# Optimization experiments

Hardware: AMD Instinct MI355X
Metric: run time of the kernel (lower is better)

Reference implementation:

```python
import jax, jax.numpy as jnp
import numpy as np

THRESH = 0.5   # global `thresh` used by ActFun
LENS = 0.5     # global `lens` (surrogate width)
DECAY = 0.25   # LIFNode init_decay
INV_STD = 1.0 / float(np.sqrt(1.0 + 1e-5))  # BN eval: running_mean=0, running_var=1
HEADS = 8
WINDOW = 8

@jax.custom_vjp
def act_fun(x):
    return (x > THRESH).astype(x.dtype)

def _act_fwd(x):
    return act_fun(x), x

def _act_bwd(x, g):
    temp = (jnp.abs(x - THRESH) < LENS).astype(g.dtype) / (2.0 * LENS)
    return (g * temp,)

act_fun.defvjp(_act_fwd, _act_bwd)

def lif(x):
    # x: [T, ...]; mem = x[0]; mem_t = mem_{t-1}*decay*(1-spike_{t-1}.detach()) + x_t
    spike0 = act_fun(x[0])
    def step(carry, xi):
        mem_prev, spike_prev = carry
        mem = mem_prev * DECAY * (1.0 - jax.lax.stop_gradient(spike_prev)) + xi
        spike = act_fun(mem)
        return (mem, spike), spike
    _, spikes = jax.lax.scan(step, (x[0], spike0), x[1:])
    return jnp.concatenate([spike0[None], spikes], axis=0)

def bn_eval(x, gamma, beta):
    # BatchNorm2d eval over channel D (last dim of [T,B,L,D]) with default running stats
    return x * (INV_STD * gamma) + beta

def linear(x, w, b):
    # torch nn.Linear: y = x @ w.T + b, w: [out, in]
    return jnp.einsum('tbld,ed->tble', x, w) + b


def setup_inputs() -> dict:
    key = jax.random.key(0)
    ks = jax.random.split(key, 12)
    T, B, L, D = 4, 4, 1024, 512
    s = 0.02
    inp = {
        'x': jax.random.normal(ks[0], (T, B, L, D), dtype=jnp.float32),
        'pos_bias': jax.random.uniform(ks[1], (L, L), dtype=jnp.float32),
        'q_w': jax.random.normal(ks[2], (D, D), dtype=jnp.float32) * s,
        'q_b': jnp.zeros((D,), jnp.float32),
        'q_g': jnp.ones((D,), jnp.float32),
        'q_beta': jnp.zeros((D,), jnp.float32),
        'k_w': jax.random.normal(ks[3], (D, D), dtype=jnp.float32) * s,
        'k_b': jnp.zeros((D,), jnp.float32),
        'k_g': jnp.ones((D,), jnp.float32),
        'k_beta': jnp.zeros((D,), jnp.float32),
        'v_w': jax.random.normal(ks[4], (D, D), dtype=jnp.float32) * s,
        'v_b': jnp.zeros((D,), jnp.float32),
        'v_g': jnp.ones((D,), jnp.float32),
        'v_beta': jnp.zeros((D,), jnp.float32),
        'last_w': jax.random.normal(ks[5], (D, D), dtype=jnp.float32) * s,
        'last_b': jnp.zeros((D,), jnp.float32),
        'last_g': jnp.ones((D,), jnp.float32),
        'last_beta': jnp.zeros((D,), jnp.float32),
    }
    return inp


def reference(x, pos_bias, q_w, q_b, q_g, q_beta, k_w, k_b, k_g, k_beta,
              v_w, v_b, v_g, v_beta, last_w, last_b, last_g, last_beta):
    T, B, L, D = x.shape
    H = HEADS
    Dh = D // H
    # local causal band: keep pos_bias[i,j] only where 0 <= i-j < WINDOW
    i = jnp.arange(L)[:, None]
    j = jnp.arange(L)[None, :]
    band = ((i - j) >= 0) & ((i - j) < WINDOW)
    pb = jnp.where(band, pos_bias[:L, :L], 0.0)  # [L, L]

    xs = lif(x)  # first_lif
    q = lif(bn_eval(linear(xs, q_w, q_b), q_g, q_beta))
    k = lif(bn_eval(linear(xs, k_w, k_b), k_g, k_beta))
    v = lif(bn_eval(linear(xs, v_w, v_b), v_g, v_beta))

    # [T,B,L,D] -> [T,B,L,H,Dh] -> [B,H,L,T,Dh] -> [B,H,L,T*Dh]
    qh = q.reshape(T, B, L, H, Dh).transpose(1, 3, 2, 0, 4).reshape(B, H, L, T * Dh)
    kv = (k * v).reshape(T, B, L, H, Dh).transpose(1, 3, 2, 0, 4).reshape(B, H, L, T * Dh)

    attn = jnp.einsum('ij,bhjd->bhid', pb, kv)  # local-window positional mixing
    out = qh * attn
    out = out.reshape(B, H, L, T, Dh).transpose(3, 0, 2, 1, 4).reshape(T, B, L, D)
    out = lif(out)  # attn_lif
    out = bn_eval(linear(out, last_w, last_b), last_g, last_beta)
    return out
```

## Files before the change

kernel.cpp:

```cpp
#include <hip/hip_runtime.h>
#include <stdint.h>


#define T_ 4
#define B_ 4
#define L_ 1024
#define D_ 512
#define BI_ (B_*L_)
#define M_ROWS (T_*B_*L_)
#define STRIDE4 (B_*L_*D_/4)
#define INV_STD 0.9999950000374997f
#define EPS_FLAG 1e-3f
#define LIST_CAP 5000000u

typedef unsigned int   u32;
typedef unsigned short u16;
typedef __bf16 bf16x8 __attribute__((ext_vector_type(8)));
typedef float  f32x4  __attribute__((ext_vector_type(4)));

static __device__ __forceinline__ float spike_of(float m) {
  return m > 0.5f ? 1.0f : 0.0f;
}
static __device__ __forceinline__ u16 sbits(float s) {
  return s != 0.0f ? (u16)0x3F80 : (u16)0;
}

__device__ __forceinline__ void gll16(const u16* g, void* l) {
  __builtin_amdgcn_global_load_lds(
      (const __attribute__((address_space(1))) u32*)(const void*)g,
      (__attribute__((address_space(3))) u32*)l, 16, 0, 0);
}

__global__ __launch_bounds__(256) void k_wsplit(const float* __restrict__ qw,
    const float* __restrict__ kw, const float* __restrict__ vw,
    const float* __restrict__ lw, u16* __restrict__ wsp, u32* __restrict__ cnt) {
  int idx = blockIdx.x * 256 + threadIdx.x;
  if (idx == 0) *cnt = 0;
  int mat = idx >> 16;
  int u = idx & 65535;
  const float* W = mat == 0 ? qw : mat == 1 ? kw : mat == 2 ? vw : lw;
  float4 w = ((const float4*)W)[u];
  float wv[4] = {w.x, w.y, w.z, w.w};
  u16 hb[4], lb[4];
#pragma unroll
  for (int c = 0; c < 4; ++c) {
    __bf16 h = (__bf16)wv[c];
    float r = wv[c] - (float)h;
    __bf16 lo = (__bf16)r;
    hb[c] = __builtin_bit_cast(u16, h);
    lb[c] = __builtin_bit_cast(u16, lo);
  }
  u16* base = wsp + (size_t)mat * 524288;
  ((ushort4*)base)[u]            = make_ushort4(hb[0], hb[1], hb[2], hb[3]);
  ((ushort4*)(base + 262144))[u] = make_ushort4(lb[0], lb[1], lb[2], lb[3]);
}

__global__ __launch_bounds__(256) void k_lif_first(const float* __restrict__ x,
                                                   u16* __restrict__ xsb) {
  int idx = blockIdx.x * 256 + threadIdx.x;
  if (idx >= STRIDE4) return;
  const int bi = idx >> 7, d4 = idx & 127;
  const float4* x4 = (const float4*)x;
  ushort4* o4 = (ushort4*)xsb;
  float m[4], s[4];
  float4 v = x4[idx];
  m[0] = v.x; m[1] = v.y; m[2] = v.z; m[3] = v.w;
#pragma unroll
  for (int c = 0; c < 4; ++c) s[c] = spike_of(m[c]);
  o4[(bi * 4 + 0) * 128 + d4] =
      make_ushort4(sbits(s[0]), sbits(s[1]), sbits(s[2]), sbits(s[3]));
#pragma unroll
  for (int t = 1; t < T_; ++t) {
    v = x4[idx + t * STRIDE4];
    float xv[4] = {v.x, v.y, v.z, v.w};
#pragma unroll
    for (int c = 0; c < 4; ++c) {
      m[c] = m[c] * 0.25f * (1.0f - s[c]) + xv[c];
      s[c] = spike_of(m[c]);
    }
    o4[(bi * 4 + t) * 128 + d4] =
        make_ushort4(sbits(s[0]), sbits(s[1]), sbits(s[2]), sbits(s[3]));
  }
}

__device__ __forceinline__ void gemm_core(const u16* __restrict__ Ab,
    const u16* __restrict__ Wp, int row0, int col0, int tid,
    unsigned char* sm, f32x4 (&acc)[4][4]) {
  const u16* gsrc[12];
  int loff[12];
#pragma unroll
  for (int u = 0; u < 12; ++u) {
    if (u < 4) {
      int lin = u * 4096 + tid * 16;
      int r = lin >> 7, slot = (lin >> 4) & 7, gs = slot ^ (r & 7);
      gsrc[u] = Ab + (size_t)(row0 + r) * 512 + gs * 8;
      loff[u] = lin;
    } else {
      int lin = (u - 4) * 4096 + tid * 16;
      int plane = lin >> 14, l3 = lin & 16383;
      int r = l3 >> 7, slot = (l3 >> 4) & 7, gs = slot ^ (r & 7);
      gsrc[u] = Wp + (size_t)plane * 262144 + (size_t)(col0 + r) * 512 + gs * 8;
      loff[u] = 16384 + lin;
    }
  }
  const int lane = tid & 63;
  const int wid = tid >> 6;
  const int wr = wid >> 1, wc = wid & 1;
  const int la = lane & 15, lg = lane >> 4;

  int offA[4][2], offB[2][4][2];
#pragma unroll
  for (int mi = 0; mi < 4; ++mi) {
    int r = wr * 64 + mi * 16 + la;
#pragma unroll
    for (int s = 0; s < 2; ++s)
      offA[mi][s] = r * 128 + ((s * 64 + lg * 16) ^ ((r & 7) << 4));
  }
#pragma unroll
  for (int p = 0; p < 2; ++p)
#pragma unroll
    for (int ni = 0; ni < 4; ++ni) {
      int r = wc * 64 + ni * 16 + la;
#pragma unroll
      for (int s = 0; s < 2; ++s)
        offB[p][ni][s] = 16384 + p * 16384 + r * 128 +
                         ((s * 64 + lg * 16) ^ ((r & 7) << 4));
    }

#pragma unroll
  for (int a = 0; a < 4; ++a)
#pragma unroll
    for (int b = 0; b < 4; ++b) acc[a][b] = (f32x4){0.f, 0.f, 0.f, 0.f};

  for (int k0 = 0; k0 < 8; ++k0) {
#pragma unroll
    for (int u = 0; u < 12; ++u) gll16(gsrc[u] + (k0 << 6), sm + loff[u]);
    __syncthreads();
    uint4 af[4][2];
#pragma unroll
    for (int mi = 0; mi < 4; ++mi)
#pragma unroll
      for (int s = 0; s < 2; ++s)
        af[mi][s] = *(const uint4*)(sm + offA[mi][s]);
#pragma unroll
    for (int p = 0; p < 2; ++p)
#pragma unroll
      for (int s = 0; s < 2; ++s)
#pragma unroll
        for (int ni = 0; ni < 4; ++ni) {
          uint4 bf = *(const uint4*)(sm + offB[p][ni][s]);
#pragma unroll
          for (int mi = 0; mi < 4; ++mi)
            acc[mi][ni] = __builtin_amdgcn_mfma_f32_16x16x32_bf16(
                __builtin_bit_cast(bf16x8, af[mi][s]),
                __builtin_bit_cast(bf16x8, bf), acc[mi][ni], 0, 0, 0);
        }
    __syncthreads();
  }
}

__global__ __launch_bounds__(256) void k_gemm_lif(const u16* __restrict__ Ab,
    const u16* __restrict__ Wp, const float* __restrict__ bias,
    const float* __restrict__ gamma, const float* __restrict__ beta,
    u16* __restrict__ S, u32* __restrict__ list, u32* __restrict__ cnt,
    int tz) {
  __shared__ __align__(16) unsigned char sm[49152];
  const int tid = threadIdx.x;
  int f = blockIdx.y * 4 + blockIdx.x;
  int tI = (f & 7) * 64 + (f >> 3);
  const int row0 = (tI >> 2) * 128;
  const int col0 = (tI & 3) * 128;

  f32x4 acc[4][4];
  gemm_core(Ab, Wp, row0, col0, tid, sm, acc);

  const int lane = tid & 63;
  const int wid = tid >> 6;
  const int wr = wid >> 1, wc = wid & 1;
  const int la = lane & 15, lg = lane >> 4;

#pragma unroll
  for (int ni = 0; ni < 4; ++ni) {
    int e = col0 + wc * 64 + ni * 16 + la;
    float cs = INV_STD * gamma[e];
    float cb = bias[e], ct = beta[e];
#pragma unroll
    for (int mi = 0; mi < 4; ++mi) {
      int r = row0 + wr * 64 + mi * 16 + lg * 4;
      int bi = r >> 2;
      float m = 0.f, s = 0.f;
      int fl = 0;
      u16 sb[4];
#pragma unroll
      for (int p = 0; p < 4; ++p) {
        float pre = (acc[mi][ni][p] + cb) * cs + ct;
        if (p == 0) m = pre;
        else m = m * 0.25f * (1.0f - s) + pre;
        s = spike_of(m);
        if (fabsf(m - 0.5f) < EPS_FLAG) fl = 1;
        sb[p] = sbits(s);
      }
#pragma unroll
      for (int p = 0; p < 4; ++p)
        S[(size_t)(r + p) * 512 + e] = sb[p];
      if (fl) {
        u32 pos = atomicAdd(cnt, 1u);
        if (pos < LIST_CAP)
          list[pos] = ((u32)tz << 21) | (u32)(bi * 512 + e);
      }
    }
  }
}

__global__ __launch_bounds__(256) void k_gemm_out(const u16* __restrict__ Ab,
    const u16* __restrict__ Wp, const float* __restrict__ bias,
    const float* __restrict__ gamma, const float* __restrict__ beta,
    float* __restrict__ Y) {
  __shared__ __align__(16) unsigned char sm[49152];
  const int tid = threadIdx.x;
  int f = blockIdx.y * 4 + blockIdx.x;
  int tI = (f & 7) * 64 + (f >> 3);
  const int row0 = (tI >> 2) * 128;
  const int col0 = (tI & 3) * 128;

  f32x4 acc[4][4];
  gemm_core(Ab, Wp, row0, col0, tid, sm, acc);

  const int lane = tid & 63;
  const int wid = tid >> 6;
  const int wr = wid >> 1, wc = wid & 1;
  const int la = lane & 15, lg = lane >> 4;

#pragma unroll
  for (int ni = 0; ni < 4; ++ni) {
    int e = col0 + wc * 64 + ni * 16 + la;
    float cs = INV_STD * gamma[e];
    float cb = bias[e], ct = beta[e];
#pragma unroll
    for (int mi = 0; mi < 4; ++mi) {
      int r = row0 + wr * 64 + mi * 16 + lg * 4;
      int bi = r >> 2;
#pragma unroll
      for (int p = 0; p < 4; ++p)
        Y[(size_t)(p * BI_ + bi) * 512 + e] = (acc[mi][ni][p] + cb) * cs + ct;
    }
  }
}

__device__ __forceinline__ void consume32_1(const float4 (&wb)[8],
                                            const uint4 (&ab)[4], float& c) {
#pragma unroll
  for (int u = 0; u < 8; ++u) {
    float4 w = wb[u];
    uint4 tt = ab[u >> 1];
    u32 a = (u & 1) ? tt.z : tt.x, b = (u & 1) ? tt.w : tt.y;
    c += (a & 0xFFFFu) ? w.x : 0.0f;
    c += (a >> 16)     ? w.y : 0.0f;
    c += (b & 0xFFFFu) ? w.z : 0.0f;
    c += (b >> 16)     ? w.w : 0.0f;
  }
}

__global__ __launch_bounds__(128) void k_fixup_c(const u16* __restrict__ xsb,
    u16* __restrict__ qs, u16* __restrict__ ks, u16* __restrict__ vs,
    const float* __restrict__ qw, const float* __restrict__ qb2,
    const float* __restrict__ qg, const float* __restrict__ qbe,
    const float* __restrict__ kw, const float* __restrict__ kb2,
    const float* __restrict__ kg, const float* __restrict__ kbe,
    const float* __restrict__ vw, const float* __restrict__ vb2,
    const float* __restrict__ vg, const float* __restrict__ vbe,
    const u32* __restrict__ list, const u32* __restrict__ cnt) {
  u32 n = *cnt;
  if (n > LIST_CAP) n = LIST_CAP;
  u32 tot = n * 4;
  for (u32 ii = blockIdx.x * 128 + threadIdx.x; ii < tot;
       ii += gridDim.x * 128) {
    u32 i = ii >> 2;
    int t = (int)(ii & 3);
    u32 e = list[i];
    int tz = (int)(e >> 21);
    int col = (int)(e & 0x1FFFFFu);
    int bi = col >> 9, d = col & 511;
    const float* W  = tz == 0 ? qw  : tz == 1 ? kw  : vw;
    const float* Bb = tz == 0 ? qb2 : tz == 1 ? kb2 : vb2;
    const float* Gg = tz == 0 ? qg  : tz == 1 ? kg  : vg;
    const float* Be = tz == 0 ? qbe : tz == 1 ? kbe : vbe;
    u16* S          = tz == 0 ? qs  : tz == 1 ? ks  : vs;
    const float4* w4 = (const float4*)(W + (size_t)d * 512);
    const uint4*  R  = (const uint4*)(xsb + ((size_t)bi * 4 + t) * 512);

    float4 wA[8], wB[8];
    uint4 aA[4], aB[4];
#pragma unroll
    for (int u = 0; u < 8; ++u) wA[u] = w4[u];
#pragma unroll
    for (int u = 0; u < 4; ++u) aA[u] = R[u];
    float c = 0.f;
#pragma unroll
    for (int ch = 0; ch < 16; ++ch) {
      if ((ch & 1) == 0) {
        if (ch + 1 < 16) {
          int wb0 = (ch + 1) * 8, ab0 = (ch + 1) * 4;
#pragma unroll
          for (int u = 0; u < 8; ++u) wB[u] = w4[wb0 + u];
#pragma unroll
          for (int u = 0; u < 4; ++u) aB[u] = R[ab0 + u];
        }
        consume32_1(wA, aA, c);
      } else {
        if (ch + 1 < 16) {
          int wb0 = (ch + 1) * 8, ab0 = (ch + 1) * 4;
#pragma unroll
          for (int u = 0; u < 8; ++u) wA[u] = w4[wb0 + u];
#pragma unroll
          for (int u = 0; u < 4; ++u) aA[u] = R[ab0 + u];
        }
        consume32_1(wB, aB, c);
      }
    }
    int lane = threadIdx.x & 63;
    int qb = lane & ~3;
    float cq[4];
    cq[0] = __shfl(c, qb + 0, 64);
    cq[1] = __shfl(c, qb + 1, 64);
    cq[2] = __shfl(c, qb + 2, 64);
    cq[3] = __shfl(c, qb + 3, 64);
    float cs = INV_STD * Gg[d];
    float cb = Bb[d], ct = Be[d];
    float m = 0.f, s = 0.f;
    u16 myb = 0;
#pragma unroll
    for (int t2 = 0; t2 < 4; ++t2) {
      float pre = (cq[t2] + cb) * cs + ct;
      if (t2 == 0) m = pre;
      else m = m * 0.25f * (1.0f - s) + pre;
      s = spike_of(m);
      if (t2 == t) myb = sbits(s);
    }
    S[((size_t)bi * 4 + t) * 512 + d] = myb;
  }
}

__global__ __launch_bounds__(256) void k_attn(const u16* __restrict__ qs,
    const u16* __restrict__ ks, const u16* __restrict__ vs,
    const float* __restrict__ pos_bias, u16* __restrict__ sout) {
  int idx = blockIdx.x * 256 + threadIdx.x;
  if (idx >= STRIDE4) return;
  const int d4 = idx & 127;
  const int bi = idx >> 7;
  const int i = bi & (L_ - 1);
  const int wmax = i < 7 ? i : 7;

  float pbv[8];
  const float* pbrow = pos_bias + (size_t)i * L_ + i;
  for (int w = 0; w <= wmax; ++w) pbv[w] = pbrow[-w];

  const ushort4* k4 = (const ushort4*)ks;
  const ushort4* v4 = (const ushort4*)vs;
  const ushort4* q4 = (const ushort4*)qs;
  float pre[T_][4];

#pragma unroll
  for (int t = 0; t < T_; ++t) {
    float sum[4] = {0.f, 0.f, 0.f, 0.f};
    for (int w = wmax; w >= 0; --w) {
      int rj = ((bi - w) * 4 + t) * 128 + d4;
      ushort4 ku = k4[rj];
      ushort4 vu = v4[rj];
      sum[0] += (ku.x && vu.x) ? pbv[w] : 0.0f;
      sum[1] += (ku.y && vu.y) ? pbv[w] : 0.0f;
      sum[2] += (ku.z && vu.z) ? pbv[w] : 0.0f;
      sum[3] += (ku.w && vu.w) ? pbv[w] : 0.0f;
    }
    ushort4 qu = q4[(bi * 4 + t) * 128 + d4];
    pre[t][0] = qu.x ? sum[0] : 0.0f;
    pre[t][1] = qu.y ? sum[1] : 0.0f;
    pre[t][2] = qu.z ? sum[2] : 0.0f;
    pre[t][3] = qu.w ? sum[3] : 0.0f;
  }

  ushort4* s4 = (ushort4*)sout;
  float m[4], s[4];
#pragma unroll
  for (int c = 0; c < 4; ++c) { m[c] = pre[0][c]; s[c] = spike_of(m[c]); }
  s4[(bi * 4 + 0) * 128 + d4] =
      make_ushort4(sbits(s[0]), sbits(s[1]), sbits(s[2]), sbits(s[3]));
#pragma unroll
  for (int t = 1; t < T_; ++t) {
#pragma unroll
    for (int c = 0; c < 4; ++c) {
      m[c] = m[c] * 0.25f * (1.0f - s[c]) + pre[t][c];
      s[c] = spike_of(m[c]);
    }
    s4[(bi * 4 + t) * 128 + d4] =
        make_ushort4(sbits(s[0]), sbits(s[1]), sbits(s[2]), sbits(s[3]));
  }
}

extern "C" void kernel_launch(void* const* d_in, const int* in_sizes, int n_in,
                              void* d_out, int out_size, void* d_ws, size_t ws_size,
                              hipStream_t stream) {
  (void)in_sizes; (void)n_in; (void)out_size; (void)ws_size;
  const float* x        = (const float*)d_in[0];
  const float* pos_bias = (const float*)d_in[1];
  const float* q_w    = (const float*)d_in[2];
  const float* q_b    = (const float*)d_in[3];
  const float* q_g    = (const float*)d_in[4];
  const float* q_beta = (const float*)d_in[5];
  const float* k_w    = (const float*)d_in[6];
  const float* k_b    = (const float*)d_in[7];
  const float* k_g    = (const float*)d_in[8];
  const float* k_beta = (const float*)d_in[9];
  const float* v_w    = (const float*)d_in[10];
  const float* v_b    = (const float*)d_in[11];
  const float* v_g    = (const float*)d_in[12];
  const float* v_beta = (const float*)d_in[13];
  const float* last_w    = (const float*)d_in[14];
  const float* last_b    = (const float*)d_in[15];
  const float* last_g    = (const float*)d_in[16];
  const float* last_beta = (const float*)d_in[17];
  float* out = (float*)d_out;

  char* ws = (char*)d_ws;
  u16*   xsb  = (u16*)(ws + 0);
  u16*   qs   = (u16*)(ws + 16777216);
  u16*   ks   = (u16*)(ws + 33554432);
  u16*   vs   = (u16*)(ws + 50331648);
  u16*   sA   = (u16*)(ws + 67108864);
  u16*   wsp  = (u16*)(ws + 100663296);
  u32*   list = (u32*)(ws + 104857600);
  u32*   cnt  = (u32*)(ws + 124857600);

  dim3 gg(4, 128);

  k_wsplit<<<1024, 256, 0, stream>>>(q_w, k_w, v_w, last_w, wsp, cnt);
  k_lif_first<<<2048, 256, 0, stream>>>(x, xsb);

  k_gemm_lif<<<gg, 256, 0, stream>>>(xsb, wsp + 0 * 524288, q_b, q_g, q_beta,
                                     qs, list, cnt, 0);
  k_gemm_lif<<<gg, 256, 0, stream>>>(xsb, wsp + 1 * 524288, k_b, k_g, k_beta,
                                     ks, list, cnt, 1);
  k_gemm_lif<<<gg, 256, 0, stream>>>(xsb, wsp + 2 * 524288, v_b, v_g, v_beta,
                                     vs, list, cnt, 2);

  k_fixup_c<<<2048, 128, 0, stream>>>(xsb, qs, ks, vs,
      q_w, q_b, q_g, q_beta, k_w, k_b, k_g, k_beta, v_w, v_b, v_g, v_beta,
      list, cnt);

  k_attn<<<2048, 256, 0, stream>>>(qs, ks, vs, pos_bias, sA);

  k_gemm_out<<<gg, 256, 0, stream>>>(sA, wsp + 3 * 524288,
                                     last_b, last_g, last_beta, out);
}
```

Before: 366.5 us.

## Merge Q/K/V GEMM launches and stage epilogue stores through LDS for coalescing

```diff
diff --git a/kernel.cpp b/kernel.cpp
--- a/kernel.cpp
+++ b/kernel.cpp
@@ -159,13 +159,25 @@
   }
 }
 
-__global__ __launch_bounds__(256) void k_gemm_lif(const u16* __restrict__ Ab,
-    const u16* __restrict__ Wp, const float* __restrict__ bias,
-    const float* __restrict__ gamma, const float* __restrict__ beta,
-    u16* __restrict__ S, u32* __restrict__ list, u32* __restrict__ cnt,
-    int tz) {
+__global__ __launch_bounds__(256) void k_gemm_qkv(const u16* __restrict__ Ab,
+    const u16* __restrict__ wsp,
+    const float* __restrict__ qb2, const float* __restrict__ qg,
+    const float* __restrict__ qbe,
+    const float* __restrict__ kb2, const float* __restrict__ kg,
+    const float* __restrict__ kbe,
+    const float* __restrict__ vb2, const float* __restrict__ vg,
+    const float* __restrict__ vbe,
+    u16* __restrict__ qs, u16* __restrict__ ks, u16* __restrict__ vs,
+    u32* __restrict__ list, u32* __restrict__ cnt) {
   __shared__ __align__(16) unsigned char sm[49152];
   const int tid = threadIdx.x;
+  const int tz = blockIdx.z;
+  const u16* Wp = wsp + (size_t)tz * 524288;
+  const float* Bb = tz == 0 ? qb2 : tz == 1 ? kb2 : vb2;
+  const float* Gg = tz == 0 ? qg  : tz == 1 ? kg  : vg;
+  const float* Be = tz == 0 ? qbe : tz == 1 ? kbe : vbe;
+  u16* S          = tz == 0 ? qs  : tz == 1 ? ks  : vs;
+
   int f = blockIdx.y * 4 + blockIdx.x;
   int tI = (f & 7) * 64 + (f >> 3);
   const int row0 = (tI >> 2) * 128;
@@ -179,18 +191,19 @@
   const int wr = wid >> 1, wc = wid & 1;
   const int la = lane & 15, lg = lane >> 4;
 
+  u16* sm16 = (u16*)sm;
 #pragma unroll
   for (int ni = 0; ni < 4; ++ni) {
-    int e = col0 + wc * 64 + ni * 16 + la;
-    float cs = INV_STD * gamma[e];
-    float cb = bias[e], ct = beta[e];
+    int cl = wc * 64 + ni * 16 + la;
+    int e = col0 + cl;
+    float cs = INV_STD * Gg[e];
+    float cb = Bb[e], ct = Be[e];
 #pragma unroll
     for (int mi = 0; mi < 4; ++mi) {
-      int r = row0 + wr * 64 + mi * 16 + lg * 4;
-      int bi = r >> 2;
+      int rl = wr * 64 + mi * 16 + lg * 4;
+      int bi = (row0 + rl) >> 2;
       float m = 0.f, s = 0.f;
       int fl = 0;
-      u16 sb[4];
 #pragma unroll
       for (int p = 0; p < 4; ++p) {
         float pre = (acc[mi][ni][p] + cb) * cs + ct;
@@ -198,17 +211,22 @@
         else m = m * 0.25f * (1.0f - s) + pre;
         s = spike_of(m);
         if (fabsf(m - 0.5f) < EPS_FLAG) fl = 1;
-        sb[p] = sbits(s);
+        sm16[(rl + p) * 128 + cl] = sbits(s);
       }
-#pragma unroll
-      for (int p = 0; p < 4; ++p)
-        S[(size_t)(r + p) * 512 + e] = sb[p];
       if (fl) {
         u32 pos = atomicAdd(cnt, 1u);
         if (pos < LIST_CAP)
           list[pos] = ((u32)tz << 21) | (u32)(bi * 512 + e);
       }
     }
+  }
+  __syncthreads();
+#pragma unroll
+  for (int ps = 0; ps < 8; ++ps) {
+    int rr = ps * 16 + (tid >> 4);
+    int c8 = (tid & 15) * 8;
+    uint4 vv = *(const uint4*)(sm16 + rr * 128 + c8);
+    *(uint4*)(S + (size_t)(row0 + rr) * 512 + col0 + c8) = vv;
   }
 }
 
@@ -231,19 +249,36 @@
   const int wr = wid >> 1, wc = wid & 1;
   const int la = lane & 15, lg = lane >> 4;
 
-#pragma unroll
-  for (int ni = 0; ni < 4; ++ni) {
-    int e = col0 + wc * 64 + ni * 16 + la;
-    float cs = INV_STD * gamma[e];
-    float cb = bias[e], ct = beta[e];
-#pragma unroll
-    for (int mi = 0; mi < 4; ++mi) {
-      int r = row0 + wr * 64 + mi * 16 + lg * 4;
-      int bi = r >> 2;
-#pragma unroll
-      for (int p = 0; p < 4; ++p)
-        Y[(size_t)(p * BI_ + bi) * 512 + e] = (acc[mi][ni][p] + cb) * cs + ct;
-    }
+  float* sm32 = (float*)sm;
+#pragma unroll
+  for (int h = 0; h < 2; ++h) {
+    if (wr == h) {
+#pragma unroll
+      for (int ni = 0; ni < 4; ++ni) {
+        int cl = wc * 64 + ni * 16 + la;
+        int e = col0 + cl;
+        float cs = INV_STD * gamma[e];
+        float cb = bias[e], ct = beta[e];
+#pragma unroll
+        for (int mi = 0; mi < 4; ++mi) {
+          int rb = mi * 16 + lg * 4;
+#pragma unroll
+          for (int p = 0; p < 4; ++p)
+            sm32[(rb + p) * 128 + cl] = (acc[mi][ni][p] + cb) * cs + ct;
+        }
+      }
+    }
+    __syncthreads();
+    int rl = tid >> 2;
+    int q0 = (tid & 3) * 32;
+    int gr = row0 + h * 64 + rl;
+    int bi = gr >> 2, p = gr & 3;
+    float* dst = Y + ((size_t)p * BI_ + bi) * 512 + col0 + q0;
+    const float* srcl = sm32 + rl * 128 + q0;
+#pragma unroll
+    for (int u = 0; u < 8; ++u)
+      ((uint4*)dst)[u] = ((const uint4*)srcl)[u];
+    __syncthreads();
   }
 }
 
@@ -431,17 +466,13 @@
   u32*   list = (u32*)(ws + 104857600);
   u32*   cnt  = (u32*)(ws + 124857600);
 
-  dim3 gg(4, 128);
-
   k_wsplit<<<1024, 256, 0, stream>>>(q_w, k_w, v_w, last_w, wsp, cnt);
   k_lif_first<<<2048, 256, 0, stream>>>(x, xsb);
 
-  k_gemm_lif<<<gg, 256, 0, stream>>>(xsb, wsp + 0 * 524288, q_b, q_g, q_beta,
-                                     qs, list, cnt, 0);
-  k_gemm_lif<<<gg, 256, 0, stream>>>(xsb, wsp + 1 * 524288, k_b, k_g, k_beta,
-                                     ks, list, cnt, 1);
-  k_gemm_lif<<<gg, 256, 0, stream>>>(xsb, wsp + 2 * 524288, v_b, v_g, v_beta,
-                                     vs, list, cnt, 2);
+  dim3 gq(4, 128, 3);
+  k_gemm_qkv<<<gq, 256, 0, stream>>>(xsb, wsp,
+      q_b, q_g, q_beta, k_b, k_g, k_beta, v_b, v_g, v_beta,
+      qs, ks, vs, list, cnt);
 
   k_fixup_c<<<2048, 128, 0, stream>>>(xsb, qs, ks, vs,
       q_w, q_b, q_g, q_beta, k_w, k_b, k_g, k_beta, v_w, v_b, v_g, v_beta,
@@ -449,6 +480,7 @@
 
   k_attn<<<2048, 256, 0, stream>>>(qs, ks, vs, pos_bias, sA);
 
+  dim3 gg(4, 128);
   k_gemm_out<<<gg, 256, 0, stream>>>(sA, wsp + 3 * 524288,
                                      last_b, last_g, last_beta, out);
 }
```

New measurement: 348.6 us. 4.9% less time.
